# Kernel tuning notes

Measured on AMD Instinct MI355X. Metric: run time of the kernel, lower is better.

Reference implementation:

```python
import jax, jax.numpy as jnp
import numpy as np

N = 50000
E = 500000
IN_C = 128
HEADS = 4
OUT_C = 64
EDGE_DIM = 32
NEG_SLOPE = 0.2  # PyG GATv2Conv default


def setup_inputs() -> dict:
    key = jax.random.key(0)
    ks = jax.random.split(key, 10)
    x = jax.random.normal(ks[0], (N, IN_C), dtype=jnp.float32)
    edge_index = jax.random.randint(ks[1], (2, E), 0, N, dtype=jnp.int64)
    edge_attr = jax.random.normal(ks[2], (E, EDGE_DIM), dtype=jnp.float32)
    s = 1.0 / np.sqrt(IN_C)
    W_l = jax.random.normal(ks[3], (IN_C, HEADS * OUT_C), dtype=jnp.float32) * s
    b_l = jnp.zeros((HEADS * OUT_C,), dtype=jnp.float32)
    W_r = jax.random.normal(ks[4], (IN_C, HEADS * OUT_C), dtype=jnp.float32) * s
    b_r = jnp.zeros((HEADS * OUT_C,), dtype=jnp.float32)
    W_e = jax.random.normal(ks[5], (EDGE_DIM, HEADS * OUT_C), dtype=jnp.float32) / np.sqrt(EDGE_DIM)
    att = jax.random.normal(ks[6], (HEADS, OUT_C), dtype=jnp.float32) / np.sqrt(OUT_C)
    bias = jnp.zeros((OUT_C,), dtype=jnp.float32)
    return {"x": x, "edge_index": edge_index, "edge_attr": edge_attr,
            "W_l": W_l, "b_l": b_l, "W_r": W_r, "b_r": b_r,
            "W_e": W_e, "att": att, "bias": bias}


def reference(x, edge_index, edge_attr, W_l, b_l, W_r, b_r, W_e, att, bias):
    # GATv2Conv forward (eval mode: dropout inactive), concat=False -> mean over heads
    src, dst = edge_index[0], edge_index[1]  # edge j -> i (source_to_target)
    x_l = (x @ W_l + b_l).reshape(N, HEADS, OUT_C)  # source transform
    x_r = (x @ W_r + b_r).reshape(N, HEADS, OUT_C)  # target transform
    e = (edge_attr @ W_e).reshape(E, HEADS, OUT_C)
    # per-edge score: att . LeakyReLU(x_l[j] + x_r[i] + e)
    m = x_l[src] + x_r[dst] + e                      # [E, H, C]
    m = jnp.where(m > 0, m, NEG_SLOPE * m)
    alpha = jnp.einsum('ehc,hc->eh', m, att)         # [E, H]
    # softmax over incoming edges of each target node
    amax = jax.ops.segment_max(alpha, dst, num_segments=N)   # [N, H]
    alpha = jnp.exp(alpha - amax[dst])
    denom = jax.ops.segment_sum(alpha, dst, num_segments=N)  # [N, H]
    alpha = alpha / denom[dst]
    # scatter-add weighted source messages
    out = jax.ops.segment_sum(alpha[:, :, None] * x_l[src], dst, num_segments=N)  # [N, H, C]
    out = out.mean(axis=1) + bias                    # concat=False -> mean heads
    return out
```

## Files before the change

kernel.cpp:

```cpp
#include <hip/hip_runtime.h>
#include <cstddef>

#define Nn 50000
#define Ee 500000
#define INC 128
#define HC 256
#define OUTC 64
#define EDIM 32
#define NEG 0.2f
#define NB 196

typedef __attribute__((ext_vector_type(8))) short short8;
typedef __attribute__((ext_vector_type(4))) float f32x4;

__device__ __forceinline__ unsigned short f2bf(float f) {
    unsigned u = __float_as_uint(f);
    return (unsigned short)((u + 0x7FFFu + ((u >> 16) & 1u)) >> 16);
}
__device__ __forceinline__ float bf2f(unsigned short v) {
    return __uint_as_float(((unsigned)v) << 16);
}

__device__ __forceinline__ float row_sum16(float x) {
    int i;
    i = __builtin_amdgcn_mov_dpp(__float_as_int(x), 0xB1, 0xF, 0xF, true);
    x += __int_as_float(i);
    i = __builtin_amdgcn_mov_dpp(__float_as_int(x), 0x4E, 0xF, 0xF, true);
    x += __int_as_float(i);
    i = __builtin_amdgcn_mov_dpp(__float_as_int(x), 0x141, 0xF, 0xF, true);
    x += __int_as_float(i);
    i = __builtin_amdgcn_mov_dpp(__float_as_int(x), 0x140, 0xF, 0xF, true);
    x += __int_as_float(i);
    return x;
}

__global__ __launch_bounds__(256) void pack_kernel(
    const float* __restrict__ Wl, const float* __restrict__ Wr,
    const float* __restrict__ We,
    unsigned short* __restrict__ wlf, unsigned short* __restrict__ wrf,
    unsigned short* __restrict__ wef)
{
    int sid = blockIdx.x * 256 + threadIdx.x;
    const float* W; unsigned short* dst; int s; int col; int k0;
    if (sid < 8192) {
        if (sid < 4096) { W = Wl; dst = wlf; s = sid; }
        else            { W = Wr; dst = wrf; s = sid - 4096; }
        int lane = s & 63;
        int T    = (s >> 6) & 15;
        int kc   = s >> 10;
        col = (lane & 15) * 16 + T;
        k0  = kc * 32 + (lane >> 4) * 8;
    } else if (sid < 9216) {
        W = We; dst = wef; s = sid - 8192;
        int lane = s & 63;
        int nt   = (s >> 6) & 3;
        int cb   = s >> 8;
        col = cb * 64 + (lane & 15) * 4 + nt;
        k0  = (lane >> 4) * 8;
    } else return;
    unsigned short tmp[8];
    #pragma unroll
    for (int j = 0; j < 8; ++j) tmp[j] = f2bf(W[(size_t)(k0 + j) * HC + col]);
    *(uint4*)(dst + (size_t)s * 8) = *(uint4*)tmp;
}

__global__ __launch_bounds__(256) void gemm_kernel(
    const float* __restrict__ X,
    const unsigned short* __restrict__ wlf, const float* __restrict__ bl,
    const unsigned short* __restrict__ wrf, const float* __restrict__ br,
    unsigned short* __restrict__ Ylb, unsigned short* __restrict__ Yrb)
{
    const unsigned short* wf; const float* b; unsigned short* Yb;
    if (blockIdx.y == 0) { wf = wlf; b = bl; Yb = Ylb; } else { wf = wrf; b = br; Yb = Yrb; }

    const int tid = threadIdx.x, lane = tid & 63;
    const int l15 = lane & 15, l4 = lane >> 4;
    const int r0 = blockIdx.x * 64 + (tid >> 6) * 16;

    int arow = r0 + l15; if (arow >= Nn) arow = Nn - 1;
    short8 af[4];
    #pragma unroll
    for (int kc = 0; kc < 4; ++kc) {
        const f32x4* p = (const f32x4*)(X + (size_t)arow * INC + kc * 32 + l4 * 8);
        f32x4 v0 = p[0], v1 = p[1];
        short8 a;
        a[0]=(short)f2bf(v0.x); a[1]=(short)f2bf(v0.y); a[2]=(short)f2bf(v0.z); a[3]=(short)f2bf(v0.w);
        a[4]=(short)f2bf(v1.x); a[5]=(short)f2bf(v1.y); a[6]=(short)f2bf(v1.z); a[7]=(short)f2bf(v1.w);
        af[kc] = a;
    }

    f32x4 acc[16];
    #pragma unroll
    for (int T = 0; T < 16; ++T) acc[T] = (f32x4){0.f, 0.f, 0.f, 0.f};

    #pragma unroll
    for (int kc = 0; kc < 4; ++kc) {
        #pragma unroll
        for (int T = 0; T < 16; ++T) {
            short8 bf = *(const short8*)(wf + ((size_t)(kc * 16 + T) * 64 + lane) * 8);
            acc[T] = __builtin_amdgcn_mfma_f32_16x16x32_bf16(af[kc], bf, acc[T], 0, 0, 0);
        }
    }

    float bb[16];
    #pragma unroll
    for (int t4 = 0; t4 < 4; ++t4) {
        float4 v = *(const float4*)(b + l15 * 16 + t4 * 4);
        bb[t4*4+0]=v.x; bb[t4*4+1]=v.y; bb[t4*4+2]=v.z; bb[t4*4+3]=v.w;
    }

    #pragma unroll
    for (int r = 0; r < 4; ++r) {
        int orow = r0 + l4 * 4 + r;
        if (orow < Nn) {
            unsigned short o[16];
            #pragma unroll
            for (int T = 0; T < 16; ++T) o[T] = f2bf(acc[T][r] + bb[T]);
            *(uint4*)(Yb + (size_t)orow * HC + l15 * 16)     = *(uint4*)(o);
            *(uint4*)(Yb + (size_t)orow * HC + l15 * 16 + 8) = *(uint4*)(o + 8);
        }
    }
}

__global__ __launch_bounds__(256) void zero_kernel(int* __restrict__ deg) {
    int i = blockIdx.x * 256 + threadIdx.x;
    if (i < Nn) deg[i] = 0;
}
__global__ __launch_bounds__(256) void hist_kernel(
    const int* __restrict__ ei, int* __restrict__ deg) {
    int e = blockIdx.x * 256 + threadIdx.x;
    if (e < Ee) atomicAdd(deg + ei[Ee + e], 1);
}
__global__ __launch_bounds__(256) void scan1_kernel(
    const int* __restrict__ deg, int* __restrict__ off, int* __restrict__ bsum) {
    __shared__ int s[256];
    int i = blockIdx.x * 256 + threadIdx.x;
    int v = (i < Nn) ? deg[i] : 0;
    s[threadIdx.x] = v;
    __syncthreads();
    #pragma unroll
    for (int d = 1; d < 256; d <<= 1) {
        int t = (threadIdx.x >= d) ? s[threadIdx.x - d] : 0;
        __syncthreads();
        s[threadIdx.x] += t;
        __syncthreads();
    }
    if (i < Nn) off[i] = s[threadIdx.x] - v;
    if (threadIdx.x == 255) bsum[blockIdx.x] = s[255];
}
__global__ __launch_bounds__(256) void scan2_kernel(int* __restrict__ bsum) {
    __shared__ int s[256];
    int v = (threadIdx.x < NB) ? bsum[threadIdx.x] : 0;
    s[threadIdx.x] = v;
    __syncthreads();
    #pragma unroll
    for (int d = 1; d < 256; d <<= 1) {
        int t = (threadIdx.x >= d) ? s[threadIdx.x - d] : 0;
        __syncthreads();
        s[threadIdx.x] += t;
        __syncthreads();
    }
    if (threadIdx.x < NB) bsum[threadIdx.x] = s[threadIdx.x] - v;
}
__global__ __launch_bounds__(256) void scan3_kernel(
    int* __restrict__ off, const int* __restrict__ bsum, int* __restrict__ cur) {
    int i = blockIdx.x * 256 + threadIdx.x;
    if (i < Nn) {
        int o = off[i] + bsum[blockIdx.x];
        off[i] = o;
        cur[i] = o;
    }
}
__global__ __launch_bounds__(256) void scatter_kernel(
    const int* __restrict__ ei, int* __restrict__ cur,
    int* __restrict__ csr_e, int* __restrict__ csr_s) {
    int e = blockIdx.x * 256 + threadIdx.x;
    if (e >= Ee) return;
    int d = ei[Ee + e];
    int pos = atomicAdd(cur + d, 1);
    csr_e[pos] = e;
    csr_s[pos] = ei[e];
}

__global__ __launch_bounds__(256) void edge_alpha_kernel(
    const unsigned short* __restrict__ xlb, const unsigned short* __restrict__ xrb,
    const int* __restrict__ ei, const float* __restrict__ ea,
    const unsigned short* __restrict__ wef, const float* __restrict__ att,
    float* __restrict__ alpha)
{
    const int tid  = threadIdx.x;
    const int lane = tid & 63;
    const int l15  = lane & 15, l4 = lane >> 4;
    const int e0   = blockIdx.x * 128 + (tid >> 6) * 32;

    short8 afrag[2];
    #pragma unroll
    for (int mt = 0; mt < 2; ++mt) {
        int e = e0 + mt * 16 + l15;
        if (e >= Ee) e = Ee - 1;
        const f32x4* p = (const f32x4*)(ea + (size_t)e * EDIM + l4 * 8);
        f32x4 v0 = __builtin_nontemporal_load(p);
        f32x4 v1 = __builtin_nontemporal_load(p + 1);
        short8 a;
        a[0]=(short)f2bf(v0.x); a[1]=(short)f2bf(v0.y); a[2]=(short)f2bf(v0.z); a[3]=(short)f2bf(v0.w);
        a[4]=(short)f2bf(v1.x); a[5]=(short)f2bf(v1.y); a[6]=(short)f2bf(v1.z); a[7]=(short)f2bf(v1.w);
        afrag[mt] = a;
    }

    unsigned soff[8], doff[8];
    #pragma unroll
    for (int mt = 0; mt < 2; ++mt)
        #pragma unroll
        for (int r = 0; r < 4; ++r) {
            int idx = mt * 4 + r;
            int e = e0 + mt * 16 + l4 * 4 + r;
            int ec = (e < Ee) ? e : Ee - 1;
            soff[idx] = (unsigned)ei[ec] * (unsigned)HC;
            doff[idx] = (unsigned)ei[Ee + ec] * (unsigned)HC;
        }

    #pragma unroll 1
    for (int cb = 0; cb < 4; ++cb) {
        short8 bfrag[4];
        #pragma unroll
        for (int nt = 0; nt < 4; ++nt)
            bfrag[nt] = *(const short8*)(wef + ((size_t)(cb * 4 + nt) * 64 + lane) * 8);

        f32x4 acc[2][4];
        const f32x4 z = {0.f, 0.f, 0.f, 0.f};
        #pragma unroll
        for (int mt = 0; mt < 2; ++mt)
            #pragma unroll
            for (int nt = 0; nt < 4; ++nt)
                acc[mt][nt] = __builtin_amdgcn_mfma_f32_16x16x32_bf16(
                    afrag[mt], bfrag[nt], z, 0, 0, 0);

        float4 atv = *(const float4*)(att + cb * 64 + l15 * 4);

        #pragma unroll
        for (int mt = 0; mt < 2; ++mt) {
            #pragma unroll
            for (int r = 0; r < 4; ++r) {
                const int idx = mt * 4 + r;
                const unsigned c = (unsigned)(cb * 64 + l15 * 4);
                ushort4 gl4 = *(const ushort4*)(xlb + soff[idx] + c);
                ushort4 gr4 = *(const ushort4*)(xrb + doff[idx] + c);
                float m0 = acc[mt][0][r] + bf2f(gl4.x) + bf2f(gr4.x);
                float m1 = acc[mt][1][r] + bf2f(gl4.y) + bf2f(gr4.y);
                float m2 = acc[mt][2][r] + bf2f(gl4.z) + bf2f(gr4.z);
                float m3 = acc[mt][3][r] + bf2f(gl4.w) + bf2f(gr4.w);
                m0 = fmaxf(m0, NEG * m0);
                m1 = fmaxf(m1, NEG * m1);
                m2 = fmaxf(m2, NEG * m2);
                m3 = fmaxf(m3, NEG * m3);
                float p;
                p = atv.x * m0;
                p = fmaf(atv.y, m1, p);
                p = fmaf(atv.z, m2, p);
                p = fmaf(atv.w, m3, p);
                p = row_sum16(p);
                int e = e0 + mt * 16 + l4 * 4 + r;
                if (l15 == 0 && e < Ee)
                    alpha[(size_t)e * 4 + cb] = p;
            }
        }
    }
}

__global__ __launch_bounds__(256) void node_aggr_kernel(
    const unsigned short* __restrict__ xlb,
    const int* __restrict__ csr_e, const int* __restrict__ csr_s,
    const float* __restrict__ alpha, const int* __restrict__ off,
    const int* __restrict__ deg, const float* __restrict__ bias,
    float* __restrict__ out)
{
    __shared__ float shw[4][64];
    __shared__ int   shs[4][16];
    const int lane = threadIdx.x & 63;
    const int wv   = threadIdx.x >> 6;
    const int n    = blockIdx.x * 4 + wv;
    if (n >= Nn) return;

    const int start = off[n];
    const int len   = deg[n];

    if (len == 0) {
        if (lane < 16) {
            float4 b4 = *(const float4*)(bias + lane * 4);
            *(float4*)(out + (size_t)n * OUTC + lane * 4) = b4;
        }
        return;
    }

    const int eidx = lane >> 2;
    const int hh   = lane & 3;
    const int hagg = lane >> 4;

    float m = -3.4e38f, d = 0.f;
    float4 acc = make_float4(0.f, 0.f, 0.f, 0.f);

    for (int c0 = 0; c0 < len; c0 += 16) {
        int cl = len - c0; if (cl > 16) cl = 16;
        float a = -3.4e38f;
        if (eidx < cl) {
            int e = csr_e[start + c0 + eidx];
            a = alpha[(size_t)e * 4 + hh];
        }
        if (lane < cl) shs[wv][lane] = csr_s[start + c0 + lane];
        float cm = a;
        cm = fmaxf(cm, __shfl_xor(cm, 4, 64));
        cm = fmaxf(cm, __shfl_xor(cm, 8, 64));
        cm = fmaxf(cm, __shfl_xor(cm, 16, 64));
        cm = fmaxf(cm, __shfl_xor(cm, 32, 64));
        float mn = fmaxf(m, cm);
        float sc = __expf(m - mn);
        float w  = (eidx < cl) ? __expf(a - mn) : 0.f;
        float ws = w;
        ws += __shfl_xor(ws, 4, 64);
        ws += __shfl_xor(ws, 8, 64);
        ws += __shfl_xor(ws, 16, 64);
        ws += __shfl_xor(ws, 32, 64);
        d = d * sc + ws;
        m = mn;
        shw[wv][lane] = w;
        float sca = __shfl(sc, hagg, 64);
        acc.x *= sca; acc.y *= sca; acc.z *= sca; acc.w *= sca;
        #pragma unroll 4
        for (int i = 0; i < cl; ++i) {
            int   si = shs[wv][i];
            float wi = shw[wv][i * 4 + hagg];
            ushort4 g = *(const ushort4*)(xlb + (size_t)si * HC + lane * 4);
            acc.x = fmaf(wi, bf2f(g.x), acc.x);
            acc.y = fmaf(wi, bf2f(g.y), acc.y);
            acc.z = fmaf(wi, bf2f(g.z), acc.z);
            acc.w = fmaf(wi, bf2f(g.w), acc.w);
        }
    }

    float dh = __shfl(d, hagg, 64);
    float di = 1.f / dh;
    float4 r;
    r.x = acc.x * di; r.y = acc.y * di; r.z = acc.z * di; r.w = acc.w * di;
    r.x += __shfl_xor(r.x, 16, 64); r.y += __shfl_xor(r.y, 16, 64);
    r.z += __shfl_xor(r.z, 16, 64); r.w += __shfl_xor(r.w, 16, 64);
    r.x += __shfl_xor(r.x, 32, 64); r.y += __shfl_xor(r.y, 32, 64);
    r.z += __shfl_xor(r.z, 32, 64); r.w += __shfl_xor(r.w, 32, 64);
    if (lane < 16) {
        float4 b4 = *(const float4*)(bias + lane * 4);
        float4 o = make_float4(b4.x + 0.25f * r.x, b4.y + 0.25f * r.y,
                               b4.z + 0.25f * r.z, b4.w + 0.25f * r.w);
        *(float4*)(out + (size_t)n * OUTC + lane * 4) = o;
    }
}

extern "C" void kernel_launch(void* const* d_in, const int* in_sizes, int n_in,
                              void* d_out, int out_size, void* d_ws, size_t ws_size,
                              hipStream_t stream)
{
    const float* x    = (const float*)d_in[0];
    const int*   ei   = (const int*)d_in[1];
    const float* ea   = (const float*)d_in[2];
    const float* Wl   = (const float*)d_in[3];
    const float* bl   = (const float*)d_in[4];
    const float* Wr   = (const float*)d_in[5];
    const float* br   = (const float*)d_in[6];
    const float* We   = (const float*)d_in[7];
    const float* att  = (const float*)d_in[8];
    const float* bias = (const float*)d_in[9];
    float* out = (float*)d_out;

    unsigned short* xlb   = (unsigned short*)d_ws;
    unsigned short* xrb   = xlb + (size_t)Nn * HC;
    float*          alpha = (float*)(xrb + (size_t)Nn * HC);
    unsigned short* wef   = (unsigned short*)(alpha + (size_t)Ee * 4);
    unsigned short* wlf   = wef + 8192;
    unsigned short* wrf   = wlf + 32768;
    int*            deg   = (int*)(wrf + 32768);
    int*            off   = deg + Nn;
    int*            cur   = off + Nn;
    int*            bsum  = cur + Nn;
    int*            csr_e = bsum + 256;
    int*            csr_s = csr_e + Ee;

    pack_kernel<<<36, 256, 0, stream>>>(Wl, Wr, We, wlf, wrf, wef);
    gemm_kernel<<<dim3((Nn + 63) / 64, 2), 256, 0, stream>>>(x, wlf, bl, wrf, br, xlb, xrb);
    zero_kernel<<<NB, 256, 0, stream>>>(deg);
    hist_kernel<<<(Ee + 255) / 256, 256, 0, stream>>>(ei, deg);
    scan1_kernel<<<NB, 256, 0, stream>>>(deg, off, bsum);
    scan2_kernel<<<1, 256, 0, stream>>>(bsum);
    scan3_kernel<<<NB, 256, 0, stream>>>(off, bsum, cur);
    scatter_kernel<<<(Ee + 255) / 256, 256, 0, stream>>>(ei, cur, csr_e, csr_s);
    edge_alpha_kernel<<<(Ee + 127) / 128, 256, 0, stream>>>(xlb, xrb, ei, ea, wef, att, alpha);
    node_aggr_kernel<<<(Nn + 3) / 4, 256, 0, stream>>>(xlb, csr_e, csr_s, alpha, off, deg, bias, out);
}
```

Before: 233.6 us.

## Compute edge scores in CSR order so aggregation reads alpha contiguously

The edge-score kernel now walks edges in destination-sorted CSR order. It reads source, destination and edge id from CSR arrays, which the scatter kernel now also fills with destination ids, and writes alpha indexed by CSR position. The node aggregation kernel then reads alpha contiguously instead of gathering through csr_e. In exchange, edge_attr rows become a random gather, scatter writes an extra array, and consecutive edges share a destination, which may improve xr cache reuse.

```diff
diff --git a/kernel.cpp b/kernel.cpp
--- a/kernel.cpp
+++ b/kernel.cpp
@@ -173,34 +173,37 @@
 }
 __global__ __launch_bounds__(256) void scatter_kernel(
     const int* __restrict__ ei, int* __restrict__ cur,
-    int* __restrict__ csr_e, int* __restrict__ csr_s) {
+    int* __restrict__ csr_e, int* __restrict__ csr_s, int* __restrict__ csr_d) {
     int e = blockIdx.x * 256 + threadIdx.x;
     if (e >= Ee) return;
     int d = ei[Ee + e];
     int pos = atomicAdd(cur + d, 1);
     csr_e[pos] = e;
     csr_s[pos] = ei[e];
+    csr_d[pos] = d;
 }
 
 __global__ __launch_bounds__(256) void edge_alpha_kernel(
     const unsigned short* __restrict__ xlb, const unsigned short* __restrict__ xrb,
-    const int* __restrict__ ei, const float* __restrict__ ea,
+    const int* __restrict__ csr_e, const int* __restrict__ csr_s,
+    const int* __restrict__ csr_d, const float* __restrict__ ea,
     const unsigned short* __restrict__ wef, const float* __restrict__ att,
     float* __restrict__ alpha)
 {
     const int tid  = threadIdx.x;
     const int lane = tid & 63;
     const int l15  = lane & 15, l4 = lane >> 4;
-    const int e0   = blockIdx.x * 128 + (tid >> 6) * 32;
+    const int p0   = blockIdx.x * 128 + (tid >> 6) * 32;
 
     short8 afrag[2];
     #pragma unroll
     for (int mt = 0; mt < 2; ++mt) {
-        int e = e0 + mt * 16 + l15;
-        if (e >= Ee) e = Ee - 1;
-        const f32x4* p = (const f32x4*)(ea + (size_t)e * EDIM + l4 * 8);
-        f32x4 v0 = __builtin_nontemporal_load(p);
-        f32x4 v1 = __builtin_nontemporal_load(p + 1);
+        int p = p0 + mt * 16 + l15;
+        if (p >= Ee) p = Ee - 1;
+        int e = csr_e[p];
+        const f32x4* pp = (const f32x4*)(ea + (size_t)e * EDIM + l4 * 8);
+        f32x4 v0 = __builtin_nontemporal_load(pp);
+        f32x4 v1 = __builtin_nontemporal_load(pp + 1);
         short8 a;
         a[0]=(short)f2bf(v0.x); a[1]=(short)f2bf(v0.y); a[2]=(short)f2bf(v0.z); a[3]=(short)f2bf(v0.w);
         a[4]=(short)f2bf(v1.x); a[5]=(short)f2bf(v1.y); a[6]=(short)f2bf(v1.z); a[7]=(short)f2bf(v1.w);
@@ -213,10 +216,10 @@
         #pragma unroll
         for (int r = 0; r < 4; ++r) {
             int idx = mt * 4 + r;
-            int e = e0 + mt * 16 + l4 * 4 + r;
-            int ec = (e < Ee) ? e : Ee - 1;
-            soff[idx] = (unsigned)ei[ec] * (unsigned)HC;
-            doff[idx] = (unsigned)ei[Ee + ec] * (unsigned)HC;
+            int p = p0 + mt * 16 + l4 * 4 + r;
+            int pc = (p < Ee) ? p : Ee - 1;
+            soff[idx] = (unsigned)csr_s[pc] * (unsigned)HC;
+            doff[idx] = (unsigned)csr_d[pc] * (unsigned)HC;
         }
 
     #pragma unroll 1
@@ -259,9 +262,9 @@
                 p = fmaf(atv.z, m2, p);
                 p = fmaf(atv.w, m3, p);
                 p = row_sum16(p);
-                int e = e0 + mt * 16 + l4 * 4 + r;
-                if (l15 == 0 && e < Ee)
-                    alpha[(size_t)e * 4 + cb] = p;
+                int pp = p0 + mt * 16 + l4 * 4 + r;
+                if (l15 == 0 && pp < Ee)
+                    alpha[(size_t)pp * 4 + cb] = p;
             }
         }
     }
@@ -269,7 +272,7 @@
 
 __global__ __launch_bounds__(256) void node_aggr_kernel(
     const unsigned short* __restrict__ xlb,
-    const int* __restrict__ csr_e, const int* __restrict__ csr_s,
+    const int* __restrict__ csr_s,
     const float* __restrict__ alpha, const int* __restrict__ off,
     const int* __restrict__ deg, const float* __restrict__ bias,
     float* __restrict__ out)
@@ -293,7 +296,6 @@
     }
 
     const int eidx = lane >> 2;
-    const int hh   = lane & 3;
     const int hagg = lane >> 4;
 
     float m = -3.4e38f, d = 0.f;
@@ -301,11 +303,7 @@
 
     for (int c0 = 0; c0 < len; c0 += 16) {
         int cl = len - c0; if (cl > 16) cl = 16;
-        float a = -3.4e38f;
-        if (eidx < cl) {
-            int e = csr_e[start + c0 + eidx];
-            a = alpha[(size_t)e * 4 + hh];
-        }
+        float a = (eidx < cl) ? alpha[(size_t)(start + c0) * 4 + lane] : -3.4e38f;
         if (lane < cl) shs[wv][lane] = csr_s[start + c0 + lane];
         float cm = a;
         cm = fmaxf(cm, __shfl_xor(cm, 4, 64));
@@ -381,6 +379,7 @@
     int*            bsum  = cur + Nn;
     int*            csr_e = bsum + 256;
     int*            csr_s = csr_e + Ee;
+    int*            csr_d = csr_s + Ee;
 
     pack_kernel<<<36, 256, 0, stream>>>(Wl, Wr, We, wlf, wrf, wef);
     gemm_kernel<<<dim3((Nn + 63) / 64, 2), 256, 0, stream>>>(x, wlf, bl, wrf, br, xlb, xrb);
@@ -389,7 +388,7 @@
     scan1_kernel<<<NB, 256, 0, stream>>>(deg, off, bsum);
     scan2_kernel<<<1, 256, 0, stream>>>(bsum);
     scan3_kernel<<<NB, 256, 0, stream>>>(off, bsum, cur);
-    scatter_kernel<<<(Ee + 255) / 256, 256, 0, stream>>>(ei, cur, csr_e, csr_s);
-    edge_alpha_kernel<<<(Ee + 127) / 128, 256, 0, stream>>>(xlb, xrb, ei, ea, wef, att, alpha);
-    node_aggr_kernel<<<(Nn + 3) / 4, 256, 0, stream>>>(xlb, csr_e, csr_s, alpha, off, deg, bias, out);
-}
+    scatter_kernel<<<(Ee + 255) / 256, 256, 0, stream>>>(ei, cur, csr_e, csr_s, csr_d);
+    edge_alpha_kernel<<<(Ee + 127) / 128, 256, 0, stream>>>(xlb, xrb, csr_e, csr_s, csr_d, ea, wef, att, alpha);
+    node_aggr_kernel<<<(Nn + 3) / 4, 256, 0, stream>>>(xlb, csr_s, alpha, off, deg, bias, out);
+}
```

Result: faster. 228.6 us (-2.1%).
